# Kernel optimization log

Hardware: AMD Instinct MI355X
Metric: run time of the kernel (lower is better)

The kernel has to match this reference:

```python
import jax, jax.numpy as jnp
import numpy as np

EMB_DIM = 1024
N_HEADS = 16
HEAD_DIM = EMB_DIM // N_HEADS
WINDOW = 128
B, T = 4, 2048


def setup_inputs() -> dict:
    key = jax.random.key(0)
    k1, k2, k3 = jax.random.split(key, 3)
    x = jax.random.normal(k1, (B, T, EMB_DIM), dtype=jnp.float32)
    # nn.Linear weights: stored as [out, in], applied as x @ W^T
    s1 = 1.0 / np.sqrt(EMB_DIM)
    w_qkv = jax.random.uniform(k2, (3 * EMB_DIM, EMB_DIM), jnp.float32, -s1, s1)
    w_out = jax.random.uniform(k3, (EMB_DIM, EMB_DIM), jnp.float32, -s1, s1)
    return {"x": x, "w_qkv": w_qkv, "w_out": w_out}


def reference(x, w_qkv, w_out):
    Bs, Ts, C = x.shape
    scale = HEAD_DIM ** -0.5
    qkv = x @ w_qkv.T                                   # [B,T,3C]
    qkv = qkv.reshape(Bs, Ts, 3, N_HEADS, HEAD_DIM)
    qkv = jnp.transpose(qkv, (2, 0, 3, 1, 4))           # [3,B,H,T,D]
    q, k, v = qkv[0], qkv[1], qkv[2]
    scores = jnp.einsum('bhtd,bhsd->bhts', q, k) * scale  # [B,H,T,T]
    i = jnp.arange(Ts)[:, None]
    j = jnp.arange(Ts)[None, :]
    # causal AND within sliding window: i - WINDOW <= j <= i
    allowed = (j <= i) & (j >= i - WINDOW)               # [T,T] bool
    scores = jnp.where(allowed[None, None], scores, -jnp.inf)
    attn = jax.nn.softmax(scores, axis=-1)
    out = jnp.einsum('bhts,bhsd->bhtd', attn, v)         # [B,H,T,D]
    out = jnp.transpose(out, (0, 2, 1, 3)).reshape(Bs, Ts, C)
    return out @ w_out.T
```

## Files before the change

kernel.cpp:

```cpp
#include <hip/hip_runtime.h>
#include <hip/hip_bf16.h>
#include <stdint.h>

typedef __attribute__((ext_vector_type(8))) short bf16x8;
typedef __attribute__((ext_vector_type(4))) float f32x4;
typedef __attribute__((ext_vector_type(4))) unsigned short u16x4;

#define B_ 4
#define T_ 2048
#define C_ 1024
#define H_ 16
#define D_ 64

__device__ __forceinline__ unsigned short f2bf(float f) {
  union { float f; uint32_t u; } v; v.f = f;
  uint32_t u = v.u;
  uint32_t r = (u + 0x7FFFu + ((u >> 16) & 1u)) >> 16;
  return (unsigned short)r;
}

__device__ __forceinline__ void gload_lds16(const unsigned short* g, short* l) {
  __builtin_amdgcn_global_load_lds((__attribute__((address_space(1))) void*)(uintptr_t)g,
                                   (__attribute__((address_space(3))) void*)l, 16, 0, 0);
}

__global__ void __launch_bounds__(256) cast3_f32_bf16(const float* __restrict__ x,
                                                      const float* __restrict__ wq,
                                                      const float* __restrict__ wo,
                                                      unsigned short* __restrict__ xb,
                                                      unsigned short* __restrict__ wqb,
                                                      unsigned short* __restrict__ wob) {
  int i = blockIdx.x * 256 + threadIdx.x;
  const float* s; unsigned short* d; int off;
  if (i < 2097152) { s = x; d = xb; off = i; }
  else if (i < 2097152 + 786432) { s = wq; d = wqb; off = i - 2097152; }
  else { s = wo; d = wob; off = i - 2883584; }
  float4 f = ((const float4*)s)[off];
  u16x4 o;
  o[0] = f2bf(f.x); o[1] = f2bf(f.y); o[2] = f2bf(f.z); o[3] = f2bf(f.w);
  ((u16x4*)d)[off] = o;
}

template <int MODE>
__global__ void __launch_bounds__(256) gemm_bt(const unsigned short* __restrict__ A,
                                               const unsigned short* __restrict__ Bm,
                                               unsigned short* __restrict__ qb,
                                               unsigned short* __restrict__ kb,
                                               unsigned short* __restrict__ vb,
                                               float* __restrict__ fo) {
  __shared__ short As[128 * 32];
  __shared__ short Bs[128 * 32];
  const int tid = threadIdx.x;
  const int bm = blockIdx.y * 128;
  const int bn = blockIdx.x * 128;
  const int w = tid >> 6;
  const int l = tid & 63;
  const int wm = w >> 1, wn = w & 1;
  const int lm = l & 15, lq = l >> 4;

  const int srow = w * 16 + (l >> 2);
  const int scol = (l & 3) * 8;
  const unsigned short* gA0 = A + (size_t)(bm + srow) * 1024 + scol;
  const unsigned short* gA1 = gA0 + (size_t)64 * 1024;
  const unsigned short* gB0 = Bm + (size_t)(bn + srow) * 1024 + scol;
  const unsigned short* gB1 = gB0 + (size_t)64 * 1024;
  short* dA0 = As + w * 512;
  short* dA1 = As + 2048 + w * 512;
  short* dB0 = Bs + w * 512;
  short* dB1 = Bs + 2048 + w * 512;

  f32x4 acc[4][4];
#pragma unroll
  for (int i = 0; i < 4; i++)
#pragma unroll
    for (int j = 0; j < 4; j++) acc[i][j] = (f32x4){0.f, 0.f, 0.f, 0.f};

  for (int k0 = 0; k0 < 1024; k0 += 32) {
    __syncthreads();
    gload_lds16(gA0 + k0, dA0);
    gload_lds16(gA1 + k0, dA1);
    gload_lds16(gB0 + k0, dB0);
    gload_lds16(gB1 + k0, dB1);
    __syncthreads();
    bf16x8 af[4], bfr[4];
#pragma unroll
    for (int i = 0; i < 4; i++)
      af[i] = *(const bf16x8*)&As[(wm * 64 + 16 * i + lm) * 32 + 8 * lq];
#pragma unroll
    for (int j = 0; j < 4; j++)
      bfr[j] = *(const bf16x8*)&Bs[(wn * 64 + 16 * j + lm) * 32 + 8 * lq];
#pragma unroll
    for (int i = 0; i < 4; i++)
#pragma unroll
      for (int j = 0; j < 4; j++)
        acc[i][j] = __builtin_amdgcn_mfma_f32_16x16x32_bf16(af[i], bfr[j], acc[i][j], 0, 0, 0);
  }

#pragma unroll
  for (int i = 0; i < 4; i++) {
#pragma unroll
    for (int j = 0; j < 4; j++) {
#pragma unroll
      for (int r = 0; r < 4; r++) {
        int m = bm + wm * 64 + 16 * i + 4 * lq + r;
        int n = bn + wn * 64 + 16 * j + lm;
        float val = acc[i][j][r];
        if (MODE == 0) {
          int which = n >> 10, rem = n & 1023;
          int h = rem >> 6, d = rem & 63;
          int b = m >> 11, t = m & 2047;
          if (which == 0) val *= 0.1803368801f;
          unsigned short* dst = (which == 0) ? qb : ((which == 1) ? kb : vb);
          dst[(((size_t)(b * 16 + h)) * 2048 + t) * 64 + d] = f2bf(val);
        } else {
          fo[(size_t)m * 1024 + n] = val;
        }
      }
    }
  }
}

__global__ void __launch_bounds__(256) transpose_v(const unsigned short* __restrict__ Vb,
                                                   unsigned short* __restrict__ Vt) {
  __shared__ unsigned short Ls[64 * 66];
  const int tid = threadIdx.x;
  const int bh = blockIdx.y;
  const int t0 = blockIdx.x * 64;
  const size_t base = (size_t)bh * (T_ * D_);
  const int d0 = (tid & 7) * 8;
  const int it = tid >> 3;
#pragma unroll
  for (int p = 0; p < 2; p++) {
    int t = it + 32 * p;
    bf16x8 v = *(const bf16x8*)(Vb + base + (size_t)(t0 + t) * 64 + d0);
#pragma unroll
    for (int e = 0; e < 8; e++) Ls[(d0 + e) * 66 + t] = (unsigned short)v[e];
  }
  __syncthreads();
  const int d = tid >> 2;
  const int c = tid & 3;
  uint32_t r[8];
  const uint32_t* Lw = (const uint32_t*)&Ls[d * 66 + c * 16];
#pragma unroll
  for (int wj = 0; wj < 8; wj++) r[wj] = Lw[wj];
  unsigned short* o = Vt + base + (size_t)d * T_ + t0 + c * 16;
  *(uint4*)o = *(const uint4*)&r[0];
  *(uint4*)(o + 8) = *(const uint4*)&r[4];
}

__global__ void __launch_bounds__(256) attn_swa(const unsigned short* __restrict__ Qb,
                                               const unsigned short* __restrict__ Kb,
                                               const unsigned short* __restrict__ Vt,
                                               unsigned short* __restrict__ Ob) {
  __shared__ short P[4][5][16 * 40];
  const int wv = threadIdx.x >> 6;
  const int l = threadIdx.x & 63;
  const int wid = blockIdx.x * 4 + wv;
  const int bh = wid >> 7;
  const int t0 = (wid & 127) << 4;
  const int lm = l & 15, lq = l >> 4;
  const size_t base = (size_t)bh * (T_ * D_);

  bf16x8 aq0 = *(const bf16x8*)(Qb + base + (size_t)(t0 + lm) * 64 + 8 * lq);
  bf16x8 aq1 = *(const bf16x8*)(Qb + base + (size_t)(t0 + lm) * 64 + 32 + 8 * lq);

  const int j0b = t0 - 144;
  float sv[5][8];

#pragma unroll
  for (int c = 0; c < 5; c++) {
    int j0 = j0b + 32 * c;
#pragma unroll
    for (int hh = 0; hh < 2; hh++) {
      int kr = j0 + 16 * hh + lm; if (kr < 0) kr = 0;
      const unsigned short* kp = Kb + base + (size_t)kr * 64;
      bf16x8 b0 = *(const bf16x8*)(kp + 8 * lq);
      bf16x8 b1 = *(const bf16x8*)(kp + 32 + 8 * lq);
      f32x4 s = (f32x4){0.f, 0.f, 0.f, 0.f};
      s = __builtin_amdgcn_mfma_f32_16x16x32_bf16(aq0, b0, s, 0, 0, 0);
      s = __builtin_amdgcn_mfma_f32_16x16x32_bf16(aq1, b1, s, 0, 0, 0);
#pragma unroll
      for (int r = 0; r < 4; r++) sv[c][hh * 4 + r] = s[r];
    }
  }

  float lsum[4];
#pragma unroll
  for (int r = 0; r < 4; r++) {
    int t = t0 + 4 * lq + r;
    int lo = t - 128; if (lo < 0) lo = 0;
    float m2 = -1e30f;
#pragma unroll
    for (int c = 0; c < 5; c++)
#pragma unroll
      for (int hh = 0; hh < 2; hh++) {
        int j = j0b + 32 * c + 16 * hh + lm;
        float s = (j >= lo && j <= t) ? sv[c][hh * 4 + r] : -1e30f;
        sv[c][hh * 4 + r] = s;
        m2 = fmaxf(m2, s);
      }
#pragma unroll
    for (int off = 1; off < 16; off <<= 1) m2 = fmaxf(m2, __shfl_xor(m2, off));
    float ls = 0.f;
#pragma unroll
    for (int c = 0; c < 5; c++)
#pragma unroll
      for (int hh = 0; hh < 2; hh++) {
        float p = __builtin_amdgcn_exp2f(sv[c][hh * 4 + r] - m2);
        sv[c][hh * 4 + r] = p;
        ls += p;
      }
#pragma unroll
    for (int off = 1; off < 16; off <<= 1) ls += __shfl_xor(ls, off);
    lsum[r] = ls;
  }

#pragma unroll
  for (int c = 0; c < 5; c++)
#pragma unroll
    for (int r = 0; r < 4; r++)
#pragma unroll
      for (int hh = 0; hh < 2; hh++)
        P[wv][c][(4 * lq + r) * 40 + 16 * hh + lm] = (short)f2bf(sv[c][hh * 4 + r]);

  f32x4 Oa[4];
#pragma unroll
  for (int jt = 0; jt < 4; jt++) Oa[jt] = (f32x4){0.f, 0.f, 0.f, 0.f};
#pragma unroll
  for (int c = 0; c < 5; c++) {
    bf16x8 pa = *(const bf16x8*)&P[wv][c][lm * 40 + 8 * lq];
    int tb = j0b + 32 * c + 8 * lq; if (tb < 0) tb = 0;
#pragma unroll
    for (int jt = 0; jt < 4; jt++) {
      bf16x8 vf = *(const bf16x8*)(Vt + base + (size_t)(16 * jt + lm) * T_ + tb);
      Oa[jt] = __builtin_amdgcn_mfma_f32_16x16x32_bf16(pa, vf, Oa[jt], 0, 0, 0);
    }
  }

  const int b = bh >> 4, h = bh & 15;
#pragma unroll
  for (int r = 0; r < 4; r++) {
    float inv = 1.0f / lsum[r];
    int t = t0 + 4 * lq + r;
#pragma unroll
    for (int jt = 0; jt < 4; jt++) {
      int cc = h * 64 + 16 * jt + lm;
      Ob[((size_t)(b * T_ + t)) * 1024 + cc] = f2bf(Oa[jt][r] * inv);
    }
  }
}

extern "C" void kernel_launch(void* const* d_in, const int* in_sizes, int n_in,
                              void* d_out, int out_size, void* d_ws, size_t ws_size,
                              hipStream_t stream) {
  const float* x = (const float*)d_in[0];
  const float* w_qkv = (const float*)d_in[1];
  const float* w_out = (const float*)d_in[2];
  float* out = (float*)d_out;

  unsigned short* xb = (unsigned short*)d_ws;
  unsigned short* wqkvb = xb + (size_t)8192 * 1024;
  unsigned short* woutb = wqkvb + (size_t)3072 * 1024;
  unsigned short* qb = woutb + (size_t)1024 * 1024;
  unsigned short* kb = qb + (size_t)64 * 2048 * 64;
  unsigned short* vb = kb + (size_t)64 * 2048 * 64;
  unsigned short* vtb = xb;
  unsigned short* ob = vb;

  cast3_f32_bf16<<<12288, 256, 0, stream>>>(x, w_qkv, w_out, xb, wqkvb, woutb);
  gemm_bt<0><<<dim3(24, 64), 256, 0, stream>>>(xb, wqkvb, qb, kb, vb, nullptr);
  transpose_v<<<dim3(32, 64), 256, 0, stream>>>(vb, vtb);
  attn_swa<<<2048, 256, 0, stream>>>(qb, kb, vtb, ob);
  gemm_bt<1><<<dim3(8, 64), 256, 0, stream>>>(ob, woutb, nullptr, nullptr, nullptr, out);
}
```

Before: 240.0 us.

## Fuse V transpose into QKV GEMM epilogue and move softmax scaling into attention

```diff
diff --git a/kernel.cpp b/kernel.cpp
--- a/kernel.cpp
+++ b/kernel.cpp
@@ -41,13 +41,11 @@
   ((u16x4*)d)[off] = o;
 }
 
-template <int MODE>
-__global__ void __launch_bounds__(256) gemm_bt(const unsigned short* __restrict__ A,
-                                               const unsigned short* __restrict__ Bm,
-                                               unsigned short* __restrict__ qb,
-                                               unsigned short* __restrict__ kb,
-                                               unsigned short* __restrict__ vb,
-                                               float* __restrict__ fo) {
+__global__ void __launch_bounds__(256) gemm_qkv(const unsigned short* __restrict__ A,
+                                                const unsigned short* __restrict__ Bm,
+                                                unsigned short* __restrict__ qb,
+                                                unsigned short* __restrict__ kb,
+                                                unsigned short* __restrict__ vtb) {
   __shared__ short As[128 * 32];
   __shared__ short Bs[128 * 32];
   const int tid = threadIdx.x;
@@ -96,56 +94,112 @@
         acc[i][j] = __builtin_amdgcn_mfma_f32_16x16x32_bf16(af[i], bfr[j], acc[i][j], 0, 0, 0);
   }
 
-#pragma unroll
-  for (int i = 0; i < 4; i++) {
-#pragma unroll
-    for (int j = 0; j < 4; j++) {
+  if (blockIdx.x < 16) {
+#pragma unroll
+    for (int i = 0; i < 4; i++) {
+#pragma unroll
+      for (int j = 0; j < 4; j++) {
+#pragma unroll
+        for (int r = 0; r < 4; r++) {
+          int m = bm + wm * 64 + 16 * i + 4 * lq + r;
+          int n = bn + wn * 64 + 16 * j + lm;
+          int which = n >> 10, rem = n & 1023;
+          int h = rem >> 6, d = rem & 63;
+          int b = m >> 11, t = m & 2047;
+          unsigned short* dst = (which == 0) ? qb : kb;
+          dst[(((size_t)(b * 16 + h)) * 2048 + t) * 64 + d] = f2bf(acc[i][j][r]);
+        }
+      }
+    }
+  } else {
+    __syncthreads();
+    short* Lw = (w < 2) ? (As + w * 1280) : (Bs + (w - 2) * 1280);
+    const int h = ((bn - 2048) >> 6) + wn;
+    const int b = bm >> 11;
+    const int tbase = (bm & 2047) + wm * 64;
+    unsigned short* vrow = vtb + ((size_t)(b * 16 + h) * 64 + l) * 2048 + tbase;
+#pragma unroll
+    for (int i = 0; i < 4; i++) {
+#pragma unroll
+      for (int j = 0; j < 4; j++)
+#pragma unroll
+        for (int r = 0; r < 4; r++)
+          Lw[(16 * j + lm) * 20 + 4 * lq + r] = (short)f2bf(acc[i][j][r]);
+      const short* rp = &Lw[l * 20];
+      uint2 a0 = *(const uint2*)(rp + 0);
+      uint2 a1 = *(const uint2*)(rp + 4);
+      uint2 a2 = *(const uint2*)(rp + 8);
+      uint2 a3 = *(const uint2*)(rp + 12);
+      uint4 s0; s0.x = a0.x; s0.y = a0.y; s0.z = a1.x; s0.w = a1.y;
+      uint4 s1; s1.x = a2.x; s1.y = a2.y; s1.z = a3.x; s1.w = a3.y;
+      unsigned short* dst = vrow + 16 * i;
+      *(uint4*)(dst) = s0;
+      *(uint4*)(dst + 8) = s1;
+    }
+  }
+}
+
+__global__ void __launch_bounds__(256) gemm_out(const unsigned short* __restrict__ A,
+                                                const unsigned short* __restrict__ Bm,
+                                                float* __restrict__ fo) {
+  __shared__ short As[128 * 32];
+  __shared__ short Bs[128 * 32];
+  const int tid = threadIdx.x;
+  const int bm = blockIdx.y * 128;
+  const int bn = blockIdx.x * 128;
+  const int w = tid >> 6;
+  const int l = tid & 63;
+  const int wm = w >> 1, wn = w & 1;
+  const int lm = l & 15, lq = l >> 4;
+
+  const int srow = w * 16 + (l >> 2);
+  const int scol = (l & 3) * 8;
+  const unsigned short* gA0 = A + (size_t)(bm + srow) * 1024 + scol;
+  const unsigned short* gA1 = gA0 + (size_t)64 * 1024;
+  const unsigned short* gB0 = Bm + (size_t)(bn + srow) * 1024 + scol;
+  const unsigned short* gB1 = gB0 + (size_t)64 * 1024;
+  short* dA0 = As + w * 512;
+  short* dA1 = As + 2048 + w * 512;
+  short* dB0 = Bs + w * 512;
+  short* dB1 = Bs + 2048 + w * 512;
+
+  f32x4 acc[4][4];
+#pragma unroll
+  for (int i = 0; i < 4; i++)
+#pragma unroll
+    for (int j = 0; j < 4; j++) acc[i][j] = (f32x4){0.f, 0.f, 0.f, 0.f};
+
+  for (int k0 = 0; k0 < 1024; k0 += 32) {
+    __syncthreads();
+    gload_lds16(gA0 + k0, dA0);
+    gload_lds16(gA1 + k0, dA1);
+    gload_lds16(gB0 + k0, dB0);
+    gload_lds16(gB1 + k0, dB1);
+    __syncthreads();
+    bf16x8 af[4], bfr[4];
+#pragma unroll
+    for (int i = 0; i < 4; i++)
+      af[i] = *(const bf16x8*)&As[(wm * 64 + 16 * i + lm) * 32 + 8 * lq];
+#pragma unroll
+    for (int j = 0; j < 4; j++)
+      bfr[j] = *(const bf16x8*)&Bs[(wn * 64 + 16 * j + lm) * 32 + 8 * lq];
+#pragma unroll
+    for (int i = 0; i < 4; i++)
+#pragma unroll
+      for (int j = 0; j < 4; j++)
+        acc[i][j] = __builtin_amdgcn_mfma_f32_16x16x32_bf16(af[i], bfr[j], acc[i][j], 0, 0, 0);
+  }
+
+#pragma unroll
+  for (int i = 0; i < 4; i++)
+#pragma unroll
+    for (int j = 0; j < 4; j++)
 #pragma unroll
       for (int r = 0; r < 4; r++) {
         int m = bm + wm * 64 + 16 * i + 4 * lq + r;
         int n = bn + wn * 64 + 16 * j + lm;
-        float val = acc[i][j][r];
-        if (MODE == 0) {
-          int which = n >> 10, rem = n & 1023;
-          int h = rem >> 6, d = rem & 63;
-          int b = m >> 11, t = m & 2047;
-          if (which == 0) val *= 0.1803368801f;
-          unsigned short* dst = (which == 0) ? qb : ((which == 1) ? kb : vb);
-          dst[(((size_t)(b * 16 + h)) * 2048 + t) * 64 + d] = f2bf(val);
-        } else {
-          fo[(size_t)m * 1024 + n] = val;
-        }
+        fo[(size_t)m * 1024 + n] = acc[i][j][r];
       }
-    }
-  }
-}
-
-__global__ void __launch_bounds__(256) transpose_v(const unsigned short* __restrict__ Vb,
-                                                   unsigned short* __restrict__ Vt) {
-  __shared__ unsigned short Ls[64 * 66];
-  const int tid = threadIdx.x;
-  const int bh = blockIdx.y;
-  const int t0 = blockIdx.x * 64;
-  const size_t base = (size_t)bh * (T_ * D_);
-  const int d0 = (tid & 7) * 8;
-  const int it = tid >> 3;
-#pragma unroll
-  for (int p = 0; p < 2; p++) {
-    int t = it + 32 * p;
-    bf16x8 v = *(const bf16x8*)(Vb + base + (size_t)(t0 + t) * 64 + d0);
-#pragma unroll
-    for (int e = 0; e < 8; e++) Ls[(d0 + e) * 66 + t] = (unsigned short)v[e];
-  }
-  __syncthreads();
-  const int d = tid >> 2;
-  const int c = tid & 3;
-  uint32_t r[8];
-  const uint32_t* Lw = (const uint32_t*)&Ls[d * 66 + c * 16];
-#pragma unroll
-  for (int wj = 0; wj < 8; wj++) r[wj] = Lw[wj];
-  unsigned short* o = Vt + base + (size_t)d * T_ + t0 + c * 16;
-  *(uint4*)o = *(const uint4*)&r[0];
-  *(uint4*)(o + 8) = *(const uint4*)&r[4];
 }
 
 __global__ void __launch_bounds__(256) attn_swa(const unsigned short* __restrict__ Qb,
@@ -165,6 +219,7 @@
   bf16x8 aq1 = *(const bf16x8*)(Qb + base + (size_t)(t0 + lm) * 64 + 32 + 8 * lq);
 
   const int j0b = t0 - 144;
+  const float cs = 0.125f * 1.44269504f;
   float sv[5][8];
 
 #pragma unroll
@@ -195,7 +250,7 @@
 #pragma unroll
       for (int hh = 0; hh < 2; hh++) {
         int j = j0b + 32 * c + 16 * hh + lm;
-        float s = (j >= lo && j <= t) ? sv[c][hh * 4 + r] : -1e30f;
+        float s = (j >= lo && j <= t) ? sv[c][hh * 4 + r] * cs : -1e30f;
         sv[c][hh * 4 + r] = s;
         m2 = fmaxf(m2, s);
       }
@@ -263,13 +318,11 @@
   unsigned short* woutb = wqkvb + (size_t)3072 * 1024;
   unsigned short* qb = woutb + (size_t)1024 * 1024;
   unsigned short* kb = qb + (size_t)64 * 2048 * 64;
-  unsigned short* vb = kb + (size_t)64 * 2048 * 64;
-  unsigned short* vtb = xb;
-  unsigned short* ob = vb;
+  unsigned short* vtb = kb + (size_t)64 * 2048 * 64;
+  unsigned short* ob = xb;
 
   cast3_f32_bf16<<<12288, 256, 0, stream>>>(x, w_qkv, w_out, xb, wqkvb, woutb);
-  gemm_bt<0><<<dim3(24, 64), 256, 0, stream>>>(xb, wqkvb, qb, kb, vb, nullptr);
-  transpose_v<<<dim3(32, 64), 256, 0, stream>>>(vb, vtb);
+  gemm_qkv<<<dim3(24, 64), 256, 0, stream>>>(xb, wqkvb, qb, kb, vtb);
   attn_swa<<<2048, 256, 0, stream>>>(qb, kb, vtb, ob);
-  gemm_bt<1><<<dim3(8, 64), 256, 0, stream>>>(ob, woutb, nullptr, nullptr, nullptr, out);
-}
+  gemm_out<<<dim3(8, 64), 256, 0, stream>>>(ob, woutb, out);
+}
```

Result: slower. 296.8 us (+23.7%).
